# Kernel tuning notes

Hardware: AMD Instinct MI355X
Metric: run time of the kernel (lower is better)

## Reference

```python
import jax, jax.numpy as jnp
import numpy as np

D_MODEL = 128
N_HEADS = 8
D_FF = 2048
EPS = 1e-5


def _layernorm(x, g):
    mu = jnp.mean(x, axis=-1, keepdims=True)
    var = jnp.mean((x - mu) ** 2, axis=-1, keepdims=True)
    return (x - mu) * jax.lax.rsqrt(var + EPS) * g


def setup_inputs() -> dict:
    key = jax.random.key(0)
    ks = jax.random.split(key, 9)
    d, h, dff = D_MODEL, N_HEADS, D_FF
    s = 0.02
    return {
        "x": jax.random.normal(ks[0], (4, 2048, d), dtype=jnp.float32),
        "Wq": jax.random.normal(ks[1], (d, h * d), dtype=jnp.float32) * s,
        "Wk": jax.random.normal(ks[2], (d, h * d), dtype=jnp.float32) * s,
        "Wv": jax.random.normal(ks[3], (d, h * d), dtype=jnp.float32) * s,
        "Wo": jax.random.normal(ks[4], (h * d, d), dtype=jnp.float32) * s,
        "W1": jax.random.normal(ks[5], (d, dff), dtype=jnp.float32) * s,
        "W2": jax.random.normal(ks[6], (dff, d), dtype=jnp.float32) * s,
        "g1": jnp.ones((d,), dtype=jnp.float32),
        "g2": jnp.ones((d,), dtype=jnp.float32),
    }


def reference(x, Wq, Wk, Wv, Wo, W1, W2, g1, g2):
    b, sq, d = x.shape
    h = N_HEADS
    # projections: note head_dim == d_model in this module
    Q = (x @ Wq).reshape(b, sq, h, d).transpose(0, 2, 1, 3)  # [b,h,s,d]
    K = (x @ Wk).reshape(b, sq, h, d).transpose(0, 2, 1, 3)
    V = (x @ Wv).reshape(b, sq, h, d).transpose(0, 2, 1, 3)
    scores = jnp.einsum("bhqd,bhkd->bhqk", Q, K) / np.sqrt(d).astype(jnp.float32)
    attn = jax.nn.softmax(scores, axis=-1)
    ctx = jnp.einsum("bhqk,bhkd->bhqd", attn, V)
    ctx = ctx.transpose(0, 2, 1, 3).reshape(b, sq, h * d)
    sa = ctx @ Wo
    x = _layernorm(x + sa, g1)
    ff = jax.nn.relu(x @ W1) @ W2
    x = _layernorm(x + ff, g2)
    return x
```

## Files before the change

### kernel.cpp

```cpp
#include <hip/hip_runtime.h>
#include <stdint.h>


using f32x4 = __attribute__((ext_vector_type(4))) float;
using s16x8 = __attribute__((ext_vector_type(8))) short;
using s16x4 = __attribute__((ext_vector_type(4))) short;
typedef __bf16 bf16x8 __attribute__((ext_vector_type(8)));

__device__ inline void mfma_bf16(f32x4* acc, s16x8 a, s16x8 b) {
    *acc = __builtin_amdgcn_mfma_f32_16x16x32_bf16(
        __builtin_bit_cast(bf16x8, a), __builtin_bit_cast(bf16x8, b), *acc, 0, 0, 0);
}

__device__ inline short f2bf(float f) {
    uint32_t u = __builtin_bit_cast(uint32_t, f);
    u += 0x7fffu + ((u >> 16) & 1u);
    return (short)(u >> 16);
}

__device__ inline float bf2f(short s) {
    return __builtin_bit_cast(float, (uint32_t)((uint16_t)s) << 16);
}

__device__ inline void gload16(const short* g, short* l) {
    __builtin_amdgcn_global_load_lds(
        (const __attribute__((address_space(1))) void*)g,
        (__attribute__((address_space(3))) void*)l, 16, 0, 0);
}

__global__ __launch_bounds__(256) void k_transpose_all(
    const float* __restrict__ Wq, const float* __restrict__ Wk,
    const float* __restrict__ Wv, const float* __restrict__ Wo,
    const float* __restrict__ W1, const float* __restrict__ W2,
    short* __restrict__ WqT, short* __restrict__ WkT, short* __restrict__ WvT,
    short* __restrict__ WoT, short* __restrict__ W1T, short* __restrict__ W2T)
{
    int b = blockIdx.x;
    const float* w; short* wt; int R, lc, lb;
    if (b < 512)       { w = Wq; wt = WqT; R = 128;  lc = 10; lb = 0;    }
    else if (b < 1024) { w = Wk; wt = WkT; R = 128;  lc = 10; lb = 512;  }
    else if (b < 1536) { w = Wv; wt = WvT; R = 128;  lc = 10; lb = 1024; }
    else if (b < 2048) { w = Wo; wt = WoT; R = 1024; lc = 7;  lb = 1536; }
    else if (b < 3072) { w = W1; wt = W1T; R = 128;  lc = 11; lb = 2048; }
    else               { w = W2; wt = W2T; R = 2048; lc = 7;  lb = 3072; }
    int i = (b - lb) * 256 + threadIdx.x;
    int r = i >> lc, c = i & ((1 << lc) - 1);
    wt[c * R + r] = f2bf(w[i]);
}

__global__ __launch_bounds__(256) void k_qkv(
    const float* __restrict__ xPair, const short* __restrict__ WqT,
    const short* __restrict__ WkT, const short* __restrict__ WvT,
    short* __restrict__ Qh, short* __restrict__ Kh, short* __restrict__ Vt)
{
    __shared__ __align__(16) short Bls[64 * 128];
    const int z = blockIdx.z;
    const int bt = blockIdx.y >> 4;
    const int n0 = (blockIdx.y & 15) * 64;
    const short* __restrict__ WT = (z == 0) ? WqT : (z == 1) ? WkT : WvT;
    const int w = threadIdx.x >> 6, lane = threadIdx.x & 63;
    const int g = lane >> 4, li = lane & 15;
    const int m0 = blockIdx.x * 64 + w * 16;
    const float* __restrict__ xB = xPair + (size_t)bt * 2048 * 128;

    #pragma unroll
    for (int c2 = 0; c2 < 4; ++c2) {
        int ci = c2 * 256 + (int)threadIdx.x;
        int row = ci >> 4, cc = ci & 15;
        gload16(WT + (size_t)(n0 + row) * 128 + ((cc ^ (row & 7)) * 8),
                &Bls[(c2 * 256 + w * 64) * 8]);
    }
    __syncthreads();

    f32x4 acc[4] = {};
    #pragma unroll
    for (int ks = 0; ks < 4; ++ks) {
        const float* xr = xB + (size_t)(m0 + li) * 128 + ks * 32 + g * 8;
        float4 v0 = *(const float4*)xr, v1 = *(const float4*)(xr + 4);
        s16x8 a = { f2bf(v0.x), f2bf(v0.y), f2bf(v0.z), f2bf(v0.w),
                    f2bf(v1.x), f2bf(v1.y), f2bf(v1.z), f2bf(v1.w) };
        #pragma unroll
        for (int nt = 0; nt < 4; ++nt) {
            s16x8 bfr = *(const s16x8*)&Bls[(nt * 16 + li) * 128
                                            + (((ks * 4 + g) ^ (li & 7)) * 8)];
            mfma_bf16(&acc[nt], a, bfr);
        }
    }
    const float sc = (z == 0) ? 0.12751879524622257f : 1.0f;
    #pragma unroll
    for (int nt = 0; nt < 4; ++nt) {
        int col = n0 + nt * 16 + li;
        int hh = col >> 7, dd = col & 127;
        int bh = bt * 8 + hh;
        if (z == 2) {
            int row0 = m0 + g * 4;
            int kt = row0 >> 6, so = row0 & 63;
            s16x4 o = { f2bf(acc[nt][0]), f2bf(acc[nt][1]),
                        f2bf(acc[nt][2]), f2bf(acc[nt][3]) };
            *(s16x4*)(Vt + (((size_t)bh * 32 + kt) * 128 + dd) * 64 + so) = o;
        } else {
            short* __restrict__ dst = (z == 0) ? Qh : Kh;
            #pragma unroll
            for (int r = 0; r < 4; ++r)
                dst[((size_t)bh * 2048 + m0 + g * 4 + r) * 128 + dd] =
                    f2bf(acc[nt][r] * sc);
        }
    }
}

__global__ __launch_bounds__(512) void k_attn(
    const short* __restrict__ Qh, const short* __restrict__ Kh,
    const short* __restrict__ Vt, short* __restrict__ O)
{
    __shared__ __align__(16) short Kls[2][64 * 128];
    __shared__ __align__(16) short Vls[2][128 * 64];
    __shared__ __align__(16) short Pls[8][16 * 64];
    const int hh = blockIdx.y;
    const int bt = blockIdx.z;
    const int bh = bt * 8 + hh;
    const size_t base  = (size_t)bh * 2048 * 128;
    const size_t vbase = (size_t)bh * 32 * 8192;
    const int w = threadIdx.x >> 6, lane = threadIdx.x & 63;
    const int g = lane >> 4, li = lane & 15;
    const int q0 = blockIdx.x * 128;
    const int qw = q0 + w * 16;

    #define STAGE(BUF, KT)                                                      \
        { _Pragma("unroll")                                                     \
          for (int c2 = 0; c2 < 2; ++c2) {                                      \
              int ci = c2 * 512 + (int)threadIdx.x;                             \
              int row = ci >> 4, cc = ci & 15;                                  \
              gload16(Kh + base + (size_t)((KT) * 64 + row) * 128               \
                         + ((cc ^ (row & 7)) * 8),                              \
                      &Kls[BUF][(c2 * 512 + w * 64) * 8]);                      \
              int d = ci >> 3, jc = ci & 7;                                     \
              gload16(Vt + vbase + (size_t)(KT) * 8192 + d * 64                 \
                         + ((jc ^ (d & 7)) * 8),                                \
                      &Vls[BUF][(c2 * 512 + w * 64) * 8]);                      \
          } }

    s16x8 qf[4];
    #pragma unroll
    for (int ks = 0; ks < 4; ++ks)
        qf[ks] = *(const s16x8*)(Qh + base + (size_t)(qw + li) * 128 + ks * 32 + g * 8);

    f32x4 acc[8] = {};
    float mrow[4] = { -1e30f, -1e30f, -1e30f, -1e30f };
    float lpart[4] = { 0.f, 0.f, 0.f, 0.f };

    STAGE(0, 0);
    for (int t = 0; t < 32; ++t) {
        const int cur = t & 1;
        __syncthreads();
        if (t + 1 < 32) STAGE(cur ^ 1, t + 1);

        f32x4 st[4];
        __builtin_amdgcn_s_setprio(1);
        #pragma unroll
        for (int nt = 0; nt < 4; ++nt) {
            st[nt] = (f32x4){0.f, 0.f, 0.f, 0.f};
            #pragma unroll
            for (int ks = 0; ks < 4; ++ks) {
                s16x8 bfr = *(const s16x8*)&Kls[cur][(nt * 16 + li) * 128
                                                + (((ks * 4 + g) ^ (li & 7)) * 8)];
                mfma_bf16(&st[nt], qf[ks], bfr);
            }
        }
        __builtin_amdgcn_s_setprio(0);

        float mxl[4];
        bool cond = true;
        #pragma unroll
        for (int r = 0; r < 4; ++r) {
            mxl[r] = fmaxf(fmaxf(st[0][r], st[1][r]), fmaxf(st[2][r], st[3][r]));
            cond = cond && (mxl[r] <= mrow[r] + 8.f);
        }
        if (__all(cond)) {
            #pragma unroll
            for (int r = 0; r < 4; ++r) {
                float rs = 0.f;
                #pragma unroll
                for (int nt = 0; nt < 4; ++nt) {
                    float p = exp2f(st[nt][r] - mrow[r]);
                    st[nt][r] = p;
                    rs += p;
                }
                lpart[r] += rs;
            }
        } else {
            #pragma unroll
            for (int r = 0; r < 4; ++r) {
                float mx = mxl[r];
                mx = fmaxf(mx, __shfl_xor(mx, 1));
                mx = fmaxf(mx, __shfl_xor(mx, 2));
                mx = fmaxf(mx, __shfl_xor(mx, 4));
                mx = fmaxf(mx, __shfl_xor(mx, 8));
                float mnew = fmaxf(mrow[r], mx);
                float alpha = exp2f(mrow[r] - mnew);
                float rs = 0.f;
                #pragma unroll
                for (int nt = 0; nt < 4; ++nt) {
                    float p = exp2f(st[nt][r] - mnew);
                    st[nt][r] = p;
                    rs += p;
                }
                lpart[r] = lpart[r] * alpha + rs;
                mrow[r] = mnew;
                #pragma unroll
                for (int dt = 0; dt < 8; ++dt) acc[dt][r] *= alpha;
            }
        }

        short* pw = Pls[w];
        #pragma unroll
        for (int nt = 0; nt < 4; ++nt)
            #pragma unroll
            for (int r = 0; r < 4; ++r) {
                int row = g * 4 + r;
                pw[row * 64 + (((nt * 2 + (li >> 3)) ^ (row & 7)) * 8) + (li & 7)]
                    = f2bf(st[nt][r]);
            }
        __builtin_amdgcn_s_setprio(1);
        #pragma unroll
        for (int kk = 0; kk < 2; ++kk) {
            s16x8 af = *(const s16x8*)&pw[li * 64 + (((kk * 4 + g) ^ (li & 7)) * 8)];
            #pragma unroll
            for (int dt = 0; dt < 8; ++dt) {
                s16x8 bfr = *(const s16x8*)&Vls[cur][(dt * 16 + li) * 64
                                                + (((kk * 4 + g) ^ (li & 7)) * 8)];
                mfma_bf16(&acc[dt], af, bfr);
            }
        }
        __builtin_amdgcn_s_setprio(0);
    }
    #undef STAGE

    #pragma unroll
    for (int r = 0; r < 4; ++r) {
        float rs = lpart[r];
        rs += __shfl_xor(rs, 1);
        rs += __shfl_xor(rs, 2);
        rs += __shfl_xor(rs, 4);
        rs += __shfl_xor(rs, 8);
        float inv = 1.f / rs;
        size_t row = (size_t)bt * 2048 + q0 + w * 16 + g * 4 + r;
        #pragma unroll
        for (int dt = 0; dt < 8; ++dt)
            O[row * 1024 + hh * 128 + dt * 16 + li] = f2bf(acc[dt][r] * inv);
    }
}

__global__ __launch_bounds__(256) void k_oproj(
    const short* __restrict__ O, const short* __restrict__ WoT,
    const float* __restrict__ resid, const float* __restrict__ gain,
    float* __restrict__ outp)
{
    __shared__ float red[3][16 * 128];
    const int w = threadIdx.x >> 6, lane = threadIdx.x & 63;
    const int g = lane >> 4, li = lane & 15;
    const int m0 = blockIdx.x * 16;
    const int row = m0 + li;
    f32x4 acc[8] = {};
    #pragma unroll
    for (int kq = 0; kq < 8; ++kq) {
        int ks = w * 8 + kq;
        s16x8 a = *(const s16x8*)(O + (size_t)row * 1024 + ks * 32 + g * 8);
        #pragma unroll
        for (int nt = 0; nt < 8; ++nt) {
            s16x8 bfr = *(const s16x8*)(WoT + (size_t)(nt * 16 + li) * 1024
                                           + ks * 32 + g * 8);
            mfma_bf16(&acc[nt], a, bfr);
        }
    }
    if (w > 0) {
        #pragma unroll
        for (int nt = 0; nt < 8; ++nt)
            #pragma unroll
            for (int r = 0; r < 4; ++r)
                red[w - 1][(g * 4 + r) * 128 + nt * 16 + li] = acc[nt][r];
    }
    __syncthreads();
    if (w == 0) {
        float gv[8];
        #pragma unroll
        for (int nt = 0; nt < 8; ++nt) gv[nt] = gain[nt * 16 + li];
        #pragma unroll
        for (int r = 0; r < 4; ++r) {
            int orow = m0 + g * 4 + r;
            float s = 0.f, s2 = 0.f;
            #pragma unroll
            for (int nt = 0; nt < 8; ++nt) {
                float v = acc[nt][r]
                        + red[0][(g * 4 + r) * 128 + nt * 16 + li]
                        + red[1][(g * 4 + r) * 128 + nt * 16 + li]
                        + red[2][(g * 4 + r) * 128 + nt * 16 + li]
                        + resid[(size_t)orow * 128 + nt * 16 + li];
                acc[nt][r] = v;
                s += v; s2 += v * v;
            }
            s  += __shfl_xor(s, 1);  s  += __shfl_xor(s, 2);
            s  += __shfl_xor(s, 4);  s  += __shfl_xor(s, 8);
            s2 += __shfl_xor(s2, 1); s2 += __shfl_xor(s2, 2);
            s2 += __shfl_xor(s2, 4); s2 += __shfl_xor(s2, 8);
            float mean = s * (1.f / 128.f);
            float var  = s2 * (1.f / 128.f) - mean * mean;
            float rstd = rsqrtf(var + 1e-5f);
            #pragma unroll
            for (int nt = 0; nt < 8; ++nt)
                outp[(size_t)orow * 128 + nt * 16 + li] =
                    (acc[nt][r] - mean) * rstd * gv[nt];
        }
    }
}

__global__ __launch_bounds__(256) void k_ffn(
    const float* __restrict__ x1, const short* __restrict__ W1T,
    const short* __restrict__ W2T, const float* __restrict__ gain,
    float* __restrict__ outp)
{
    __shared__ __align__(16) short hls[4][2][16 * 64];
    __shared__ float red[3][2][16 * 128];
    const int w = threadIdx.x >> 6, lane = threadIdx.x & 63;
    const int g = lane >> 4, li = lane & 15;
    const size_t m0 = (size_t)blockIdx.y * 2048 + blockIdx.x * 32;
    s16x8 xf[2][4];
    #pragma unroll
    for (int mt = 0; mt < 2; ++mt)
        #pragma unroll
        for (int ks = 0; ks < 4; ++ks) {
            const float* xr = x1 + (m0 + mt * 16 + li) * 128 + ks * 32 + g * 8;
            float4 v0 = *(const float4*)xr, v1 = *(const float4*)(xr + 4);
            xf[mt][ks] = (s16x8){ f2bf(v0.x), f2bf(v0.y), f2bf(v0.z), f2bf(v0.w),
                                  f2bf(v1.x), f2bf(v1.y), f2bf(v1.z), f2bf(v1.w) };
        }
    f32x4 acc[2][8] = {};
    #pragma unroll 2
    for (int cq = 0; cq < 8; ++cq) {
        int ch = w * 8 + cq;
        f32x4 st[2][4] = {};
        #pragma unroll
        for (int nt = 0; nt < 4; ++nt)
            #pragma unroll
            for (int ks = 0; ks < 4; ++ks) {
                s16x8 bfr = *(const s16x8*)(W1T + (size_t)(ch * 64 + nt * 16 + li) * 128
                                               + ks * 32 + g * 8);
                mfma_bf16(&st[0][nt], xf[0][ks], bfr);
                mfma_bf16(&st[1][nt], xf[1][ks], bfr);
            }
        #pragma unroll
        for (int mt = 0; mt < 2; ++mt) {
            short* hw = hls[w][mt];
            #pragma unroll
            for (int nt = 0; nt < 4; ++nt)
                #pragma unroll
                for (int r = 0; r < 4; ++r) {
                    int rw = g * 4 + r;
                    hw[rw * 64 + (((nt * 2 + (li >> 3)) ^ (rw & 7)) * 8) + (li & 7)]
                        = f2bf(fmaxf(st[mt][nt][r], 0.f));
                }
        }
        #pragma unroll
        for (int kk = 0; kk < 2; ++kk) {
            s16x8 af0 = *(const s16x8*)&hls[w][0][li * 64
                                                  + (((kk * 4 + g) ^ (li & 7)) * 8)];
            s16x8 af1 = *(const s16x8*)&hls[w][1][li * 64
                                                  + (((kk * 4 + g) ^ (li & 7)) * 8)];
            #pragma unroll
            for (int nt = 0; nt < 8; ++nt) {
                s16x8 bfr = *(const s16x8*)(W2T + (size_t)(nt * 16 + li) * 2048
                                               + ch * 64 + kk * 32 + g * 8);
                mfma_bf16(&acc[0][nt], af0, bfr);
                mfma_bf16(&acc[1][nt], af1, bfr);
            }
        }
    }
    if (w > 0) {
        #pragma unroll
        for (int mt = 0; mt < 2; ++mt)
            #pragma unroll
            for (int nt = 0; nt < 8; ++nt)
                #pragma unroll
                for (int r = 0; r < 4; ++r)
                    red[w - 1][mt][(g * 4 + r) * 128 + nt * 16 + li] = acc[mt][nt][r];
    }
    __syncthreads();
    if (w == 0) {
        float gv[8];
        #pragma unroll
        for (int nt = 0; nt < 8; ++nt) gv[nt] = gain[nt * 16 + li];
        #pragma unroll
        for (int mt = 0; mt < 2; ++mt)
            #pragma unroll
            for (int r = 0; r < 4; ++r) {
                size_t orow = m0 + mt * 16 + g * 4 + r;
                float s = 0.f, s2 = 0.f;
                #pragma unroll
                for (int nt = 0; nt < 8; ++nt) {
                    float v = acc[mt][nt][r]
                            + red[0][mt][(g * 4 + r) * 128 + nt * 16 + li]
                            + red[1][mt][(g * 4 + r) * 128 + nt * 16 + li]
                            + red[2][mt][(g * 4 + r) * 128 + nt * 16 + li]
                            + x1[orow * 128 + nt * 16 + li];
                    acc[mt][nt][r] = v;
                    s += v; s2 += v * v;
                }
                s  += __shfl_xor(s, 1);  s  += __shfl_xor(s, 2);
                s  += __shfl_xor(s, 4);  s  += __shfl_xor(s, 8);
                s2 += __shfl_xor(s2, 1); s2 += __shfl_xor(s2, 2);
                s2 += __shfl_xor(s2, 4); s2 += __shfl_xor(s2, 8);
                float mean = s * (1.f / 128.f);
                float var  = s2 * (1.f / 128.f) - mean * mean;
                float rstd = rsqrtf(var + 1e-5f);
                #pragma unroll
                for (int nt = 0; nt < 8; ++nt)
                    outp[orow * 128 + nt * 16 + li] =
                        (acc[mt][nt][r] - mean) * rstd * gv[nt];
            }
    }
}

extern "C" void kernel_launch(void* const* d_in, const int* in_sizes, int n_in,
                              void* d_out, int out_size, void* d_ws, size_t ws_size,
                              hipStream_t stream)
{
    const float* x  = (const float*)d_in[0];
    const float* Wq = (const float*)d_in[1];
    const float* Wk = (const float*)d_in[2];
    const float* Wv = (const float*)d_in[3];
    const float* Wo = (const float*)d_in[4];
    const float* W1 = (const float*)d_in[5];
    const float* W2 = (const float*)d_in[6];
    const float* g1 = (const float*)d_in[7];
    const float* g2 = (const float*)d_in[8];
    float* out = (float*)d_out;
    (void)in_sizes; (void)n_in; (void)out_size; (void)ws_size;

    char* basep = (char*)d_ws;
    size_t off = 0;
    auto carve = [&](size_t bytes) {
        void* q = basep + off;
        off += (bytes + 255) & ~(size_t)255;
        return q;
    };
    short*  WqT = (short*)carve(1024ull * 128 * 2);
    short*  WkT = (short*)carve(1024ull * 128 * 2);
    short*  WvT = (short*)carve(1024ull * 128 * 2);
    short*  WoT = (short*)carve(128ull * 1024 * 2);
    short*  W1T = (short*)carve(2048ull * 128 * 2);
    short*  W2T = (short*)carve(128ull * 2048 * 2);
    short*  Qh  = (short*)carve(16ull * 2048 * 128 * 2);
    short*  Kh  = (short*)carve(16ull * 2048 * 128 * 2);
    short*  Vt  = (short*)carve(16ull * 32 * 128 * 64 * 2);
    short*  O   = (short*)carve(4096ull * 1024 * 2);

    k_transpose_all<<<4096, 256, 0, stream>>>(Wq, Wk, Wv, Wo, W1, W2,
                                              WqT, WkT, WvT, WoT, W1T, W2T);

    for (int p = 0; p < 2; ++p) {
        const float* xp = x + (size_t)p * 4096 * 128;
        float* outp = out + (size_t)p * 4096 * 128;
        k_qkv<<<dim3(32, 32, 3), 256, 0, stream>>>(xp, WqT, WkT, WvT,
                                                   Qh, Kh, Vt);
        k_attn<<<dim3(16, 8, 2), 512, 0, stream>>>(Qh, Kh, Vt, O);
        k_oproj<<<256, 256, 0, stream>>>(O, WoT, xp, g1, outp);
    }

    k_ffn<<<dim3(64, 4), 256, 0, stream>>>(out, W1T, W2T, g2, out);
}
```

Measured before the change: 285.0 us.

## Fold max subtraction into MFMA init, compute row sums via MFMA, use hardware bf16 convert

The attention loop now seeds the QK^T accumulators with the negated running max, so the subtraction before exp2 disappears. It also replaces the per-lane row-sum accumulation and final shuffle reduction with an extra MFMA of P against a ones vector. Software bf16 rounding is swapped for the hardware conversion intrinsic in attention and FFN. This trims VALU work in the softmax inner loop and costs one extra MFMA per k-step. The denominator is now summed from bf16-rounded P, which changes numerics slightly but matches what is fed to PV.

```diff
diff --git a/kernel.cpp b/kernel.cpp
--- a/kernel.cpp
+++ b/kernel.cpp
@@ -16,6 +16,10 @@
     uint32_t u = __builtin_bit_cast(uint32_t, f);
     u += 0x7fffu + ((u >> 16) & 1u);
     return (short)(u >> 16);
+}
+
+__device__ inline short f2bf_hw(float f) {
+    return __builtin_bit_cast(short, (__bf16)f);
 }
 
 __device__ inline float bf2f(short s) {
@@ -144,9 +148,12 @@
     for (int ks = 0; ks < 4; ++ks)
         qf[ks] = *(const s16x8*)(Qh + base + (size_t)(qw + li) * 128 + ks * 32 + g * 8);
 
+    const s16x8 ones = { 0x3F80, 0x3F80, 0x3F80, 0x3F80,
+                         0x3F80, 0x3F80, 0x3F80, 0x3F80 };
+
     f32x4 acc[8] = {};
+    f32x4 acc_l = { 0.f, 0.f, 0.f, 0.f };
     float mrow[4] = { -1e30f, -1e30f, -1e30f, -1e30f };
-    float lpart[4] = { 0.f, 0.f, 0.f, 0.f };
 
     STAGE(0, 0);
     for (int t = 0; t < 32; ++t) {
@@ -154,18 +161,17 @@
         __syncthreads();
         if (t + 1 < 32) STAGE(cur ^ 1, t + 1);
 
-        f32x4 st[4];
+        f32x4 nm = { -mrow[0], -mrow[1], -mrow[2], -mrow[3] };
+        f32x4 st[4] = { nm, nm, nm, nm };
         __builtin_amdgcn_s_setprio(1);
         #pragma unroll
-        for (int nt = 0; nt < 4; ++nt) {
-            st[nt] = (f32x4){0.f, 0.f, 0.f, 0.f};
+        for (int nt = 0; nt < 4; ++nt)
             #pragma unroll
             for (int ks = 0; ks < 4; ++ks) {
                 s16x8 bfr = *(const s16x8*)&Kls[cur][(nt * 16 + li) * 128
                                                 + (((ks * 4 + g) ^ (li & 7)) * 8)];
                 mfma_bf16(&st[nt], qf[ks], bfr);
             }
-        }
         __builtin_amdgcn_s_setprio(0);
 
         float mxl[4];
@@ -173,20 +179,14 @@
         #pragma unroll
         for (int r = 0; r < 4; ++r) {
             mxl[r] = fmaxf(fmaxf(st[0][r], st[1][r]), fmaxf(st[2][r], st[3][r]));
-            cond = cond && (mxl[r] <= mrow[r] + 8.f);
+            cond = cond && (mxl[r] <= 8.f);
         }
         if (__all(cond)) {
             #pragma unroll
-            for (int r = 0; r < 4; ++r) {
-                float rs = 0.f;
-                #pragma unroll
-                for (int nt = 0; nt < 4; ++nt) {
-                    float p = exp2f(st[nt][r] - mrow[r]);
-                    st[nt][r] = p;
-                    rs += p;
-                }
-                lpart[r] += rs;
-            }
+            for (int r = 0; r < 4; ++r)
+                #pragma unroll
+                for (int nt = 0; nt < 4; ++nt)
+                    st[nt][r] = exp2f(st[nt][r]);
         } else {
             #pragma unroll
             for (int r = 0; r < 4; ++r) {
@@ -195,17 +195,13 @@
                 mx = fmaxf(mx, __shfl_xor(mx, 2));
                 mx = fmaxf(mx, __shfl_xor(mx, 4));
                 mx = fmaxf(mx, __shfl_xor(mx, 8));
-                float mnew = fmaxf(mrow[r], mx);
-                float alpha = exp2f(mrow[r] - mnew);
-                float rs = 0.f;
-                #pragma unroll
-                for (int nt = 0; nt < 4; ++nt) {
-                    float p = exp2f(st[nt][r] - mnew);
-                    st[nt][r] = p;
-                    rs += p;
-                }
-                lpart[r] = lpart[r] * alpha + rs;
-                mrow[r] = mnew;
+                float d = fmaxf(mx, 0.f);
+                float alpha = exp2f(-d);
+                #pragma unroll
+                for (int nt = 0; nt < 4; ++nt)
+                    st[nt][r] = exp2f(st[nt][r] - d);
+                mrow[r] += d;
+                acc_l[r] *= alpha;
                 #pragma unroll
                 for (int dt = 0; dt < 8; ++dt) acc[dt][r] *= alpha;
             }
@@ -218,12 +214,13 @@
             for (int r = 0; r < 4; ++r) {
                 int row = g * 4 + r;
                 pw[row * 64 + (((nt * 2 + (li >> 3)) ^ (row & 7)) * 8) + (li & 7)]
-                    = f2bf(st[nt][r]);
+                    = f2bf_hw(st[nt][r]);
             }
         __builtin_amdgcn_s_setprio(1);
         #pragma unroll
         for (int kk = 0; kk < 2; ++kk) {
             s16x8 af = *(const s16x8*)&pw[li * 64 + (((kk * 4 + g) ^ (li & 7)) * 8)];
+            mfma_bf16(&acc_l, af, ones);
             #pragma unroll
             for (int dt = 0; dt < 8; ++dt) {
                 s16x8 bfr = *(const s16x8*)&Vls[cur][(dt * 16 + li) * 64
@@ -237,16 +234,11 @@
 
     #pragma unroll
     for (int r = 0; r < 4; ++r) {
-        float rs = lpart[r];
-        rs += __shfl_xor(rs, 1);
-        rs += __shfl_xor(rs, 2);
-        rs += __shfl_xor(rs, 4);
-        rs += __shfl_xor(rs, 8);
-        float inv = 1.f / rs;
+        float inv = 1.f / acc_l[r];
         size_t row = (size_t)bt * 2048 + q0 + w * 16 + g * 4 + r;
         #pragma unroll
         for (int dt = 0; dt < 8; ++dt)
-            O[row * 1024 + hh * 128 + dt * 16 + li] = f2bf(acc[dt][r] * inv);
+            O[row * 1024 + hh * 128 + dt * 16 + li] = f2bf_hw(acc[dt][r] * inv);
     }
 }
 
@@ -356,7 +348,7 @@
                 for (int r = 0; r < 4; ++r) {
                     int rw = g * 4 + r;
                     hw[rw * 64 + (((nt * 2 + (li >> 3)) ^ (rw & 7)) * 8) + (li & 7)]
-                        = f2bf(fmaxf(st[mt][nt][r], 0.f));
+                        = f2bf_hw(fmaxf(st[mt][nt][r], 0.f));
                 }
         }
         #pragma unroll
```

New measurement: 275.7 us (median of 2 runs). 3.3% less time.
